# Kernel tuning notes

Measured on AMD Instinct MI355X. Metric: run time of the kernel, lower is better.

## Reference

```python
import jax, jax.numpy as jnp
import numpy as np


def conv2d(x, w, bias, stride=1, pad=0, groups=1):
    out = jax.lax.conv_general_dilated(
        x, w, (stride, stride), [(pad, pad), (pad, pad)],
        dimension_numbers=("NCHW", "OIHW", "NCHW"), feature_group_count=groups)
    return out + bias[None, :, None, None]


PATCHSIZE = [(4, 4), (8, 8)]
NEG = jnp.float32(-1e9)


def setup_inputs() -> dict:
    key = jax.random.key(0)
    ks = jax.random.split(key, 24)
    d = 128
    s = 0.05
    inp = {
        "x": jax.random.normal(ks[0], (16, d, 64, 64), jnp.float32),
        "m": jax.random.uniform(ks[1], (16, 1, 64, 64), jnp.float32),
        "depth_map": jax.random.normal(ks[2], (16, 1, 256, 256), jnp.float32),
        "wq": jax.random.normal(ks[3], (d, d, 1, 1), jnp.float32) * s,
        "bq": jax.random.normal(ks[4], (d,), jnp.float32) * s,
        "wk": jax.random.normal(ks[5], (d, d, 1, 1), jnp.float32) * s,
        "bk": jax.random.normal(ks[6], (d,), jnp.float32) * s,
        "wv": jax.random.normal(ks[7], (d, d, 1, 1), jnp.float32) * s,
        "bv": jax.random.normal(ks[8], (d,), jnp.float32) * s,
        "wvle": jax.random.normal(ks[9], (d, 1, 3, 3), jnp.float32) * s,  # depthwise
        "bvle": jax.random.normal(ks[10], (d,), jnp.float32) * s,
        "wd1": jax.random.normal(ks[11], (d, 1, 3, 3), jnp.float32) * s,
        "bd1": jax.random.normal(ks[12], (d,), jnp.float32) * s,
        "wd2": jax.random.normal(ks[13], (1, d, 3, 3), jnp.float32) * s,
        "bd2": jax.random.normal(ks[14], (1,), jnp.float32) * s,
        "wo": jax.random.normal(ks[15], (d, d, 3, 3), jnp.float32) * s,
        "bo": jax.random.normal(ks[16], (d,), jnp.float32) * s,
        "b": 2,
        "c": 128,
    }
    return inp


def _forward(x, m, depth_map, wq, bq, wk, bk, wv, bv, wvle, bvle,
             wd1, bd1, wd2, bd2, wo, bo, b, c):
    bt, _, h, w = x.shape
    t = bt // b
    d_k = c // len(PATCHSIZE)

    q_all = conv2d(x, wq, bq)
    k_all = conv2d(x, wk, bk)
    v_all = conv2d(x, wv, bv) + conv2d(x, wvle, bvle, pad=1, groups=c)
    d1 = jax.nn.relu(conv2d(depth_map, wd1, bd1, stride=2, pad=1))
    _depth = jax.nn.relu(conv2d(d1, wd2, bd2, stride=2, pad=1))  # (bt,1,h,w)

    outs = []
    for i, (width, height) in enumerate(PATCHSIZE):
        out_w, out_h = w // width, h // height
        L = t * out_h * out_w

        def patch(z, ch):
            # (b*t, ch, h, w) -> (b, L, ch*height*width)
            z = z.reshape(b, t, ch, out_h, height, out_w, width)
            return z.transpose(0, 1, 3, 5, 2, 4, 6).reshape(b, L, ch * height * width)

        mask = jnp.mean(patch(m, 1), -1) > 0.5            # (b, L) per-key mask
        dsort = jnp.sort(patch(_depth, 1), -1)            # (b, L, height*width)
        hw = height * width
        dmin, dmed, dmax = dsort[..., 0], dsort[..., (hw - 1) // 2], dsort[..., -1]

        q = patch(q_all[:, i * d_k:(i + 1) * d_k], d_k)
        k_ = patch(k_all[:, i * d_k:(i + 1) * d_k], d_k)
        v = patch(v_all[:, i * d_k:(i + 1) * d_k], d_k)

        scale = 1.0 / jnp.sqrt(jnp.float32(q.shape[-1]))
        s = jnp.einsum("bqd,bkd->bqk", q, k_) * scale     # shared QK^T

        def head(dbias):
            ss = s * jax.nn.sigmoid(dbias)[:, None, :]
            ss = jnp.where(mask[:, None, :], NEG, ss)
            return jnp.einsum("bqk,bkd->bqd", jax.nn.softmax(ss, -1), v)

        y = (head(dmed) + head(dmax) + head(dmin)) / 3.0
        y = y.reshape(b, t, out_h, out_w, d_k, height, width)
        y = y.transpose(0, 1, 4, 2, 5, 3, 6).reshape(bt, d_k, h, w)
        outs.append(y)

    out = jnp.concatenate(outs, 1)
    out = conv2d(out, wo, bo, pad=1)
    out = jnp.where(out >= 0, out, 0.2 * out)  # LeakyReLU(0.2)
    return out


def reference(x, m, depth_map, wq, bq, wk, bk, wv, bv, wvle, bvle,
              wd1, bd1, wd2, bd2, wo, bo, b, c):
    out = _forward(x, m, depth_map, wq, bq, wk, bk, wv, bv, wvle, bvle,
                   wd1, bd1, wd2, bd2, wo, bo, b, c)
    return (out, depth_map)
```

## Files before the change

### kernel.cpp

```cpp
#include <hip/hip_runtime.h>
#include <cmath>

typedef unsigned short u16;
typedef __attribute__((ext_vector_type(8))) __bf16 bf16x8;
typedef __attribute__((ext_vector_type(4))) float f32x4;

constexpr int Bb = 2, Tt = 8, Dc = 128, PIX = 4096;

__device__ inline u16 f2bf(float f) {
    unsigned u = __builtin_bit_cast(unsigned, f);
    u += 0x7fffu + ((u >> 16) & 1u);
    return (u16)(u >> 16);
}
__device__ inline float bf2f(u16 h) {
    unsigned u = ((unsigned)h) << 16;
    return __builtin_bit_cast(float, u);
}

#define GLOAD16(gp, lp) __builtin_amdgcn_global_load_lds( \
    (const __attribute__((address_space(1))) void*)(const void*)(gp), \
    (__attribute__((address_space(3))) void*)(void*)(lp), 16, 0, 0)

__device__ inline void mfma_chunk(const u16* lAs, const u16* lBs, int wave, int lane,
                                  f32x4 (&acc)[4][4])
{
    const int wm = (wave >> 1) * 64, wn = (wave & 1) * 64;
    const int fr = lane & 15;
    const int q4 = lane >> 4;
    const int sw = (q4 ^ ((fr >> 1) & 3)) * 8;
    bf16x8 av[4], bv[4];
#pragma unroll
    for (int i = 0; i < 4; ++i) av[i] = *(const bf16x8*)&lAs[(wm + i * 16 + fr) * 32 + sw];
#pragma unroll
    for (int j = 0; j < 4; ++j) bv[j] = *(const bf16x8*)&lBs[(wn + j * 16 + fr) * 32 + sw];
#pragma unroll
    for (int i = 0; i < 4; ++i)
#pragma unroll
        for (int j = 0; j < 4; ++j)
            acc[i][j] = __builtin_amdgcn_mfma_f32_16x16x32_bf16(av[i], bv[j], acc[i][j], 0, 0, 0);
}

__device__ inline void mfma_nt(const u16* A, int ldkA, const u16* B, int ldkB,
                               int kChunks, int wave, int lane,
                               u16* lAs, u16* lBs, f32x4 (&acc)[4][4])
{
    const int r = lane >> 2;
    const int kq8 = ((lane & 3) ^ ((r >> 1) & 3)) * 8;
    const u16* ga0 = A + (size_t)(wave * 32 + r) * ldkA + kq8;
    const u16* ga1 = ga0 + (size_t)16 * ldkA;
    const u16* gb0 = B + (size_t)(wave * 32 + r) * ldkB + kq8;
    const u16* gb1 = gb0 + (size_t)16 * ldkB;
    for (int kb = 0; kb < kChunks; ++kb) {
        __syncthreads();
        GLOAD16(ga0 + kb * 32, lAs + wave * 1024);
        GLOAD16(ga1 + kb * 32, lAs + wave * 1024 + 512);
        GLOAD16(gb0 + kb * 32, lBs + wave * 1024);
        GLOAD16(gb1 + kb * 32, lBs + wave * 1024 + 512);
        __syncthreads();
        mfma_chunk(lAs, lBs, wave, lane, acc);
    }
}

__global__ void k_prep(const float* __restrict__ wq, const float* __restrict__ wk,
                       const float* __restrict__ wv, const float* __restrict__ wo,
                       u16* __restrict__ Wqkv, u16* __restrict__ WoT)
{
    int idx = blockIdx.x * 256 + threadIdx.x;
    if (idx < 49152) {
        const float* w = idx < 16384 ? wq : (idx < 32768 ? wk : wv);
        Wqkv[idx] = f2bf(w[idx & 16383]);
    }
    int j = idx - 49152;
    if (j >= 0 && j < 147456) {
        int tap = j / 16384, rem = j % 16384;
        WoT[j] = f2bf(wo[(size_t)rem * 9 + tap]);
    }
}

__global__ __launch_bounds__(256) void k_xt(const float* __restrict__ x, u16* __restrict__ Xt)
{
    __shared__ float ls[128 * 65];
    const int n = blockIdx.y, pix0 = blockIdx.x * 64;
#pragma unroll
    for (int rep = 0; rep < 32; ++rep) {
        int idx = rep * 256 + threadIdx.x;
        int cin = idx >> 6, p = idx & 63;
        ls[cin * 65 + p] = x[((size_t)n * Dc + cin) * PIX + pix0 + p];
    }
    __syncthreads();
#pragma unroll
    for (int rep = 0; rep < 32; ++rep) {
        int idx = rep * 256 + threadIdx.x;
        int p = idx >> 7, cin = idx & 127;
        Xt[((size_t)n * PIX + pix0 + p) * Dc + cin] = f2bf(ls[cin * 65 + p]);
    }
}

__global__ __launch_bounds__(256) void k_qkv_mfma(const u16* __restrict__ Wqkv,
                                                  const u16* __restrict__ Xt,
                                                  const float* __restrict__ bq,
                                                  const float* __restrict__ bk,
                                                  const float* __restrict__ bv,
                                                  u16* __restrict__ Qp0, u16* __restrict__ Kp0,
                                                  u16* __restrict__ Qp1, u16* __restrict__ Kp1,
                                                  u16* __restrict__ v_bf)
{
    __shared__ u16 lAs[4096], lBs[4096];
    const int tid = threadIdx.x, wave = tid >> 6, lane = tid & 63;
    const int mt = blockIdx.y, n = blockIdx.z, px0 = blockIdx.x * 128;
    f32x4 acc[4][4];
#pragma unroll
    for (int i = 0; i < 4; ++i)
#pragma unroll
        for (int j = 0; j < 4; ++j) acc[i][j] = (f32x4){0.f, 0.f, 0.f, 0.f};
    mfma_nt(Wqkv + (size_t)mt * 128 * 128, 128,
            Xt + ((size_t)n * PIX + px0) * 128, 128, 4, wave, lane, lAs, lBs, acc);
    const int wm = (wave >> 1) * 64, wn = (wave & 1) * 64;
    const int rb = (lane >> 4) * 4, cb = lane & 15;
    const int bi = n >> 3, ti = n & 7;
    if (mt < 2) {
        const float* bp = (mt == 0) ? bq : bk;
        u16* d0 = (mt == 0) ? Qp0 : Kp0;
        u16* d1 = (mt == 0) ? Qp1 : Kp1;
#pragma unroll
        for (int i = 0; i < 4; ++i)
#pragma unroll
            for (int reg = 0; reg < 4; ++reg) {
                int c = wm + i * 16 + rb + reg;
                float bias = bp[c];
#pragma unroll
                for (int j = 0; j < 4; ++j) {
                    int pix = px0 + wn + j * 16 + cb;
                    int y = pix >> 6, x = pix & 63;
                    u16 val = f2bf(acc[i][j][reg] + bias);
                    if (c < 64) {
                        int l = ti * 256 + (y >> 2) * 16 + (x >> 2);
                        int f = c * 16 + (y & 3) * 4 + (x & 3);
                        d0[((size_t)bi * 2048 + l) * 1024 + f] = val;
                    } else {
                        int l = ti * 64 + (y >> 3) * 8 + (x >> 3);
                        int f = (c - 64) * 64 + (y & 7) * 8 + (x & 7);
                        d1[((size_t)bi * 512 + l) * 4096 + f] = val;
                    }
                }
            }
    } else {
#pragma unroll
        for (int i = 0; i < 4; ++i)
#pragma unroll
            for (int reg = 0; reg < 4; ++reg) {
                int c = wm + i * 16 + rb + reg;
                float bias = bv[c];
#pragma unroll
                for (int j = 0; j < 4; ++j) {
                    int pix = px0 + wn + j * 16 + cb;
                    v_bf[((size_t)n * Dc + c) * PIX + pix] = f2bf(acc[i][j][reg] + bias);
                }
            }
    }
}

__global__ __launch_bounds__(256) void k_vdw(const float* __restrict__ X,
                                             const float* __restrict__ wvle,
                                             const float* __restrict__ bvle,
                                             u16* __restrict__ v_bf)
{
    __shared__ float ls[4096];
    const int c = blockIdx.x, n = blockIdx.y;
    const int tid = threadIdx.x;
    const float* xp = X + ((size_t)n * Dc + c) * PIX;
#pragma unroll
    for (int r = 0; r < 4; ++r)
        *(float4*)&ls[r * 1024 + tid * 4] = *(const float4*)&xp[r * 1024 + tid * 4];
    __syncthreads();
    float w[9];
#pragma unroll
    for (int t = 0; t < 9; ++t) w[t] = wvle[c * 9 + t];
    const float bias = bvle[c];
    const int x = tid & 63, y0 = (tid >> 6) * 16;
    const bool xl = (x > 0), xr = (x < 63);
    u16* vp = v_bf + ((size_t)n * Dc + c) * PIX;
#pragma unroll
    for (int r = 0; r < 16; ++r) {
        int y = y0 + r;
        float s = bias;
#pragma unroll
        for (int ky = 0; ky < 3; ++ky) {
            int yy = y + ky - 1;
            if (yy < 0 || yy > 63) continue;
            const float* row = &ls[yy * 64];
            float m  = row[x];
            float lv = xl ? row[x - 1] : 0.f;
            float rv = xr ? row[x + 1] : 0.f;
            s += w[ky * 3 + 0] * lv + w[ky * 3 + 1] * m + w[ky * 3 + 2] * rv;
        }
        int idx = y * 64 + x;
        vp[idx] = f2bf(bf2f(vp[idx]) + s);
    }
}

__global__ __launch_bounds__(256) void k_d1(const float* __restrict__ dm,
                                            const float* __restrict__ wd1,
                                            const float* __restrict__ bd1,
                                            u16* __restrict__ d1b)
{
    __shared__ float ls[17 * 132];
    const int n = blockIdx.y;
    const int yt = blockIdx.x >> 1, xh = blockIdx.x & 1;
    const int Y0 = yt * 8;
    const int tid = threadIdx.x;
    const float* dmp = dm + (size_t)n * 65536;
    for (int idx = tid; idx < 17 * 132; idx += 256) {
        int row = idx / 132, cl = idx % 132;
        int gr = 2 * Y0 - 1 + row;
        int gc = 128 * xh - 1 + cl;
        float v = 0.f;
        if (gr >= 0 && gr < 256 && gc >= 0 && gc < 256 && cl < 129) v = dmp[gr * 256 + gc];
        ls[idx] = v;
    }
    __syncthreads();
    const int Xl = tid & 63;
    const int Yl0 = tid >> 6;
    float in0[9], in1[9];
#pragma unroll
    for (int jy = 0; jy < 3; ++jy)
#pragma unroll
        for (int jx = 0; jx < 3; ++jx) {
            in0[jy * 3 + jx] = ls[(2 * Yl0 + jy) * 132 + 2 * Xl + jx];
            in1[jy * 3 + jx] = ls[(2 * (Yl0 + 4) + jy) * 132 + 2 * Xl + jx];
        }
    const int X = 64 * xh + Xl;
    u16* outbase = d1b + (size_t)n * Dc * 16384 + (size_t)Y0 * 128 + X;
    for (int c = 0; c < 128; ++c) {
        const float* w1 = wd1 + c * 9;
        float a0 = bd1[c], a1 = a0;
#pragma unroll
        for (int t = 0; t < 9; ++t) { a0 += w1[t] * in0[t]; a1 += w1[t] * in1[t]; }
        u16* ob = outbase + (size_t)c * 16384;
        ob[(size_t)Yl0 * 128]       = f2bf(fmaxf(a0, 0.f));
        ob[(size_t)(Yl0 + 4) * 128] = f2bf(fmaxf(a1, 0.f));
    }
}

__global__ __launch_bounds__(256) void k_d2p(const u16* __restrict__ d1b,
                                             const float* __restrict__ wd2,
                                             float* __restrict__ part)
{
    __shared__ u16 ls[33 * 136];
    const int yt = blockIdx.x, n = blockIdx.y, cg = blockIdx.z;
    const int tid = threadIdx.x;
    const int y0 = yt * 16;
    if (tid < 33) ls[tid * 136 + 7] = 0;
    const int x = tid & 63;
    const int yl0 = (tid >> 6) * 4;
    float acc[4] = {0.f, 0.f, 0.f, 0.f};
    for (int c = 0; c < 16; ++c) {
        const u16* src = d1b + ((size_t)n * Dc + cg * 16 + c) * 16384;
        __syncthreads();
        for (int idx = tid; idx < 33 * 16; idx += 256) {
            int row = idx >> 4, s = idx & 15;
            int gr = 2 * y0 - 1 + row;
            uint4 v = make_uint4(0, 0, 0, 0);
            if (gr >= 0 && gr < 128) v = *(const uint4*)(src + gr * 128 + s * 8);
            *(uint4*)&ls[row * 136 + 8 + s * 8] = v;
        }
        __syncthreads();
        const float* w2 = wd2 + (cg * 16 + c) * 9;
        float w[9];
#pragma unroll
        for (int t = 0; t < 9; ++t) w[t] = w2[t];
#pragma unroll
        for (int r = 0; r < 4; ++r) {
            int yl = yl0 + r;
#pragma unroll
            for (int ky = 0; ky < 3; ++ky) {
                const u16* rp = &ls[(2 * yl + ky) * 136 + 2 * x + 7];
                float v0 = bf2f(rp[0]);
                unsigned pr = *(const unsigned*)(rp + 1);
                float v1 = bf2f((u16)(pr & 0xffffu));
                float v2 = bf2f((u16)(pr >> 16));
                acc[r] += w[ky * 3 + 0] * v0 + w[ky * 3 + 1] * v1 + w[ky * 3 + 2] * v2;
            }
        }
    }
    float* pp = part + ((size_t)cg * 16 + n) * PIX;
#pragma unroll
    for (int r = 0; r < 4; ++r)
        pp[(y0 + yl0 + r) * 64 + x] = acc[r];
}

__global__ void k_dfin(const float* __restrict__ part, const float* __restrict__ bd2,
                       float* __restrict__ dep)
{
    int idx = blockIdx.x * 256 + threadIdx.x;
    float s = bd2[0];
#pragma unroll
    for (int cg = 0; cg < 8; ++cg) s += part[(size_t)cg * 65536 + idx];
    dep[idx] = fmaxf(s, 0.f);
}

template<int PS>
__global__ __launch_bounds__(256) void k_stats2(const float* __restrict__ mI,
                                                const float* __restrict__ dep,
                                                float* __restrict__ maskf,
                                                float* __restrict__ smed,
                                                float* __restrict__ smaxA,
                                                float* __restrict__ sminA,
                                                int outn, int L)
{
    constexpr int HW = PS * PS;
    constexpr int TPB = 256 / HW;
    const int tok = blockIdx.x * TPB + threadIdx.x / HW;
    const int el  = threadIdx.x % HW;
    if (tok >= Bb * L) return;
    const int bi = tok / L, l = tok % L;
    const int ti = l / (outn * outn); const int rem = l % (outn * outn);
    const int oh = rem / outn, ow = rem % outn;
    const int n = bi * Tt + ti;
    const int py = el / PS, px = el % PS;
    const size_t off = (size_t)n * PIX + (size_t)(oh * PS + py) * 64 + ow * PS + px;
    const float mv = mI[off];
    const float dv = dep[off];
    float msum = mv, vmin = dv, vmax = dv;
#pragma unroll
    for (int o = HW / 2; o > 0; o >>= 1) {
        msum += __shfl_xor(msum, o);
        vmin = fminf(vmin, __shfl_xor(vmin, o));
        vmax = fmaxf(vmax, __shfl_xor(vmax, o));
    }
    const int gbase = (threadIdx.x & 63) & ~(HW - 1);
    int cl = 0, ce = 0;
#pragma unroll
    for (int b2 = 0; b2 < HW; ++b2) {
        float vb = __shfl(dv, gbase + b2);
        cl += (vb < dv);
        ce += (vb == dv);
    }
    constexpr int kk = (HW - 1) / 2;
    if (el == 0) {
        maskf[tok] = (msum / (float)HW > 0.5f) ? 1.f : 0.f;
        smaxA[tok] = 1.f / (1.f + __expf(-vmax));
        sminA[tok] = 1.f / (1.f + __expf(-vmin));
    }
    if (cl <= kk && kk < cl + ce)
        smed[tok] = 1.f / (1.f + __expf(-dv));
}

__global__ void k_patchT(const u16* __restrict__ v_bf, u16* __restrict__ Vt,
                         int ps, int outn, int L, int F, int cbase)
{
    size_t idx = (size_t)blockIdx.x * 256 + threadIdx.x;
    size_t total = (size_t)Bb * F * L / 4;
    if (idx >= total) return;
    int l0 = (int)((idx * 4) % L);
    size_t t2 = (idx * 4) / L;
    int f = (int)(t2 % F);
    int bi = (int)(t2 / F);
    int hw = ps * ps;
    int c = cbase + f / hw, r = f % hw;
    int py = r / ps, px = r % ps;
    int ti = l0 / (outn * outn); int rem = l0 % (outn * outn);
    int oh = rem / outn, ow0 = rem % outn;
    size_t base = ((size_t)(bi * Tt + ti) * Dc + c) * PIX + (oh * ps + py) * 64 + px;
    u16 out4[4];
#pragma unroll
    for (int e = 0; e < 4; ++e) out4[e] = v_bf[base + (size_t)(ow0 + e) * ps];
    *(uint2*)&Vt[((size_t)bi * F + f) * L + l0] = *(uint2*)out4;
}

__global__ __launch_bounds__(256) void k_qkT_mfma(const u16* __restrict__ Qp,
                                                  const u16* __restrict__ Kp,
                                                  u16* __restrict__ S,
                                                  int L, int F, int ksplit, float scale)
{
    __shared__ u16 lAs[4096], lBs[4096];
    const int tid = threadIdx.x, wave = tid >> 6, lane = tid & 63;
    const int bi = blockIdx.z / ksplit, ks = blockIdx.z % ksplit;
    const int kf = F / ksplit;
    f32x4 acc[4][4];
#pragma unroll
    for (int i = 0; i < 4; ++i)
#pragma unroll
        for (int j = 0; j < 4; ++j) acc[i][j] = (f32x4){0.f, 0.f, 0.f, 0.f};
    mfma_nt(Qp + (size_t)bi * L * F + (size_t)blockIdx.y * 128 * F + (size_t)ks * kf, F,
            Kp + (size_t)bi * L * F + (size_t)blockIdx.x * 128 * F + (size_t)ks * kf, F,
            kf / 32, wave, lane, lAs, lBs, acc);
    const int wm = (wave >> 1) * 64, wn = (wave & 1) * 64;
    const int rb = (lane >> 4) * 4, cb = lane & 15;
    u16* Cp = S + ((size_t)ks * Bb + bi) * L * L;
#pragma unroll
    for (int i = 0; i < 4; ++i)
#pragma unroll
        for (int reg = 0; reg < 4; ++reg) {
            int gm = blockIdx.y * 128 + wm + i * 16 + rb + reg;
#pragma unroll
            for (int j = 0; j < 4; ++j) {
                int gn = blockIdx.x * 128 + wn + j * 16 + cb;
                Cp[(size_t)gm * L + gn] = f2bf(acc[i][j][reg] * scale);
            }
        }
}

__device__ inline float blockMax(float v, float* sh) {
#pragma unroll
    for (int o = 32; o > 0; o >>= 1) v = fmaxf(v, __shfl_down(v, o));
    __syncthreads();
    if ((threadIdx.x & 63) == 0) sh[threadIdx.x >> 6] = v;
    __syncthreads();
    return fmaxf(fmaxf(sh[0], sh[1]), fmaxf(sh[2], sh[3]));
}
__device__ inline float blockSum(float v, float* sh) {
#pragma unroll
    for (int o = 32; o > 0; o >>= 1) v += __shfl_down(v, o);
    __syncthreads();
    if ((threadIdx.x & 63) == 0) sh[threadIdx.x >> 6] = v;
    __syncthreads();
    return sh[0] + sh[1] + sh[2] + sh[3];
}

template<int NV, int NSPLIT>
__global__ __launch_bounds__(256) void k_softmax(const u16* __restrict__ S,
                                                 u16* __restrict__ Pb,
                                                 const float* __restrict__ maskf,
                                                 const float* __restrict__ smed,
                                                 const float* __restrict__ smaxA,
                                                 const float* __restrict__ sminA,
                                                 int L)
{
    __shared__ float sred[4];
    const int bi = blockIdx.y, q = blockIdx.x;
    const size_t pstr = (size_t)Bb * L * L;
    const u16* row = S + (size_t)bi * L * L + (size_t)q * L;
    u16* prow = Pb + (size_t)bi * L * L + (size_t)q * L;
    const float* mk  = maskf + bi * L;
    const float* s0p = smed  + bi * L;
    const float* s1p = smaxA + bi * L;
    const float* s2p = sminA + bi * L;
    const int tid = threadIdx.x;
    float a0[NV], a1[NV], a2[NV];
    float m0 = -3.4e38f, m1 = -3.4e38f, m2 = -3.4e38f;
#pragma unroll
    for (int e = 0; e < NV; ++e) {
        int k = e * 256 + tid;
        float sv = bf2f(row[k]);
#pragma unroll
        for (int s2 = 1; s2 < NSPLIT; ++s2) sv += bf2f(row[(size_t)s2 * pstr + k]);
        bool msk = mk[k] > 0.5f;
        float v0 = msk ? -1e9f : sv * s0p[k];
        float v1 = msk ? -1e9f : sv * s1p[k];
        float v2 = msk ? -1e9f : sv * s2p[k];
        a0[e] = v0; a1[e] = v1; a2[e] = v2;
        m0 = fmaxf(m0, v0); m1 = fmaxf(m1, v1); m2 = fmaxf(m2, v2);
    }
    m0 = blockMax(m0, sred); m1 = blockMax(m1, sred); m2 = blockMax(m2, sred);
    float l0 = 0.f, l1 = 0.f, l2 = 0.f;
#pragma unroll
    for (int e = 0; e < NV; ++e) {
        a0[e] = __expf(a0[e] - m0); l0 += a0[e];
        a1[e] = __expf(a1[e] - m1); l1 += a1[e];
        a2[e] = __expf(a2[e] - m2); l2 += a2[e];
    }
    l0 = blockSum(l0, sred); l1 = blockSum(l1, sred); l2 = blockSum(l2, sred);
    float c0 = 1.f / (3.f * l0), c1 = 1.f / (3.f * l1), c2 = 1.f / (3.f * l2);
#pragma unroll
    for (int e = 0; e < NV; ++e)
        prow[e * 256 + tid] = f2bf(a0[e] * c0 + a1[e] * c1 + a2[e] * c2);
}

__global__ __launch_bounds__(256) void k_pv_mfma(const u16* __restrict__ Pb,
                                                 const u16* __restrict__ Vt,
                                                 u16* __restrict__ Yp,
                                                 int L, int F, int ksplit)
{
    __shared__ u16 lAs[4096], lBs[4096];
    const int tid = threadIdx.x, wave = tid >> 6, lane = tid & 63;
    const int bi = blockIdx.z / ksplit, ks = blockIdx.z % ksplit;
    const int kf = L / ksplit;
    f32x4 acc[4][4];
#pragma unroll
    for (int i = 0; i < 4; ++i)
#pragma unroll
        for (int j = 0; j < 4; ++j) acc[i][j] = (f32x4){0.f, 0.f, 0.f, 0.f};
    mfma_nt(Pb + (size_t)bi * L * L + (size_t)blockIdx.y * 128 * L + (size_t)ks * kf, L,
            Vt + (size_t)bi * F * L + (size_t)blockIdx.x * 128 * L + (size_t)ks * kf, L,
            kf / 32, wave, lane, lAs, lBs, acc);
    const int wm = (wave >> 1) * 64, wn = (wave & 1) * 64;
    const int rb = (lane >> 4) * 4, cb = lane & 15;
    u16* Cp = Yp + ((size_t)(ks * Bb + bi) * L) * F;
#pragma unroll
    for (int i = 0; i < 4; ++i)
#pragma unroll
        for (int reg = 0; reg < 4; ++reg) {
            int gm = blockIdx.y * 128 + wm + i * 16 + rb + reg;
#pragma unroll
            for (int j = 0; j < 4; ++j) {
                int gn = blockIdx.x * 128 + wn + j * 16 + cb;
                Cp[(size_t)gm * F + gn] = f2bf(acc[i][j][reg]);
            }
        }
}

template<int NSPLIT>
__global__ void k_unpatch(const u16* __restrict__ Yp, u16* __restrict__ catbT,
                          int ps, int outn, int L, int F, int cbase)
{
    size_t idx = (size_t)blockIdx.x * 256 + threadIdx.x;
    size_t total = (size_t)Bb * L * F / 4;
    if (idx >= total) return;
    const size_t pstr = (size_t)Bb * L * F;
    int f0 = (int)((idx * 4) % F);
    size_t t2 = (idx * 4) / F;
    int l = (int)(t2 % L);
    int bi = (int)(t2 / L);
    size_t off = ((size_t)bi * L + l) * F + f0;
    float s[4] = {0.f, 0.f, 0.f, 0.f};
#pragma unroll
    for (int sp = 0; sp < NSPLIT; ++sp) {
        uint2 u = *(const uint2*)&Yp[(size_t)sp * pstr + off];
        s[0] += bf2f((u16)(u.x & 0xffffu));
        s[1] += bf2f((u16)(u.x >> 16));
        s[2] += bf2f((u16)(u.y & 0xffffu));
        s[3] += bf2f((u16)(u.y >> 16));
    }
    int hw = ps * ps;
    int c = cbase + f0 / hw, r0 = f0 % hw;
    int ti = l / (outn * outn); int rem = l % (outn * outn);
    int oh = rem / outn, ow = rem % outn;
    int n = bi * Tt + ti;
    int py = r0 / ps, px = r0 % ps;
    size_t base = ((size_t)n * PIX + (size_t)(oh * ps + py) * 64 + ow * ps + px) * Dc + c;
#pragma unroll
    for (int e = 0; e < 4; ++e)
        catbT[base + (size_t)e * Dc] = f2bf(s[e]);
}

__global__ __launch_bounds__(256) void k_conv_mfma(const u16* __restrict__ catbT,
                                                   const u16* __restrict__ WoT,
                                                   const u16* __restrict__ zp,
                                                   u16* __restrict__ Cpart)
{
    __shared__ u16 lAs[4096], lBs[4096];
    const int tid = threadIdx.x, wave = tid >> 6, lane = tid & 63;
    const int pix0 = blockIdx.x * 128;
    const int sp = blockIdx.y;
    const int r = lane >> 2;
    const int kq8 = ((lane & 3) ^ ((r >> 1) & 3)) * 8;
    int yb[2], xb[2], nn[2];
#pragma unroll
    for (int s = 0; s < 2; ++s) {
        int pg = pix0 + wave * 32 + r + s * 16;
        nn[s] = pg >> 12; yb[s] = (pg >> 6) & 63; xb[s] = pg & 63;
    }
    const u16* gb_base = WoT + (size_t)(wave * 32 + r) * 128 + kq8;
    f32x4 acc[4][4];
#pragma unroll
    for (int i = 0; i < 4; ++i)
#pragma unroll
        for (int j = 0; j < 4; ++j) acc[i][j] = (f32x4){0.f, 0.f, 0.f, 0.f};
    for (int t = sp * 18; t < sp * 18 + 18; ++t) {
        const int tap = t >> 2, kc = t & 3;
        const int dy = tap / 3 - 1, dx = tap % 3 - 1;
        const u16* ga[2];
#pragma unroll
        for (int s = 0; s < 2; ++s) {
            int y = yb[s] + dy, xx = xb[s] + dx;
            bool ok = ((unsigned)y < 64u) && ((unsigned)xx < 64u);
            ga[s] = ok ? catbT + (((size_t)(nn[s] << 12) + y * 64 + xx) << 7) + kq8 + kc * 32 : zp;
        }
        const u16* gb = gb_base + tap * 16384 + kc * 32;
        __syncthreads();
        GLOAD16(ga[0], lAs + wave * 1024);
        GLOAD16(ga[1], lAs + wave * 1024 + 512);
        GLOAD16(gb, lBs + wave * 1024);
        GLOAD16(gb + 2048, lBs + wave * 1024 + 512);
        __syncthreads();
        mfma_chunk(lAs, lBs, wave, lane, acc);
    }
    const int wm = (wave >> 1) * 64, wn = (wave & 1) * 64;
    const int rb = (lane >> 4) * 4, cb = lane & 15;
    u16* Cp = Cpart + (size_t)sp * 8388608;
#pragma unroll
    for (int i = 0; i < 4; ++i)
#pragma unroll
        for (int reg = 0; reg < 4; ++reg) {
            int gm = pix0 + wm + i * 16 + rb + reg;
#pragma unroll
            for (int j = 0; j < 4; ++j) {
                int gn = wn + j * 16 + cb;
                Cp[(size_t)gm * 128 + gn] = f2bf(acc[i][j][reg]);
            }
        }
}

__global__ __launch_bounds__(256) void k_cfin(const u16* __restrict__ Cpart,
                                              const float* __restrict__ bo,
                                              float* __restrict__ outp)
{
    const int pg0 = blockIdx.x * 64;
    const int lane = threadIdx.x & 63, wv = threadIdx.x >> 6;
    const int pix = pg0 + lane;
    const int n = pix >> 12, p = pix & 4095;
    const u16* r0 = Cpart + (size_t)pix * 128 + wv * 32;
    const u16* r1 = r0 + 8388608;
#pragma unroll
    for (int c4 = 0; c4 < 8; ++c4) {
        uint2 a = *(const uint2*)(r0 + c4 * 4);
        uint2 b = *(const uint2*)(r1 + c4 * 4);
        float s[4];
        s[0] = bf2f((u16)(a.x & 0xffffu)) + bf2f((u16)(b.x & 0xffffu));
        s[1] = bf2f((u16)(a.x >> 16))     + bf2f((u16)(b.x >> 16));
        s[2] = bf2f((u16)(a.y & 0xffffu)) + bf2f((u16)(b.y & 0xffffu));
        s[3] = bf2f((u16)(a.y >> 16))     + bf2f((u16)(b.y >> 16));
#pragma unroll
        for (int e = 0; e < 4; ++e) {
            int cout = wv * 32 + c4 * 4 + e;
            float v = s[e] + bo[cout];
            v = (v >= 0.f) ? v : 0.2f * v;
            outp[((size_t)n * Dc + cout) * PIX + p] = v;
        }
    }
}

extern "C" void kernel_launch(void* const* d_in, const int* in_sizes, int n_in,
                              void* d_out, int out_size, void* d_ws, size_t ws_size,
                              hipStream_t stream)
{
    (void)in_sizes; (void)n_in; (void)out_size; (void)ws_size;
    const float* x    = (const float*)d_in[0];
    const float* mI   = (const float*)d_in[1];
    const float* dmap = (const float*)d_in[2];
    const float* wq   = (const float*)d_in[3];
    const float* bq   = (const float*)d_in[4];
    const float* wk   = (const float*)d_in[5];
    const float* bk   = (const float*)d_in[6];
    const float* wv   = (const float*)d_in[7];
    const float* bv   = (const float*)d_in[8];
    const float* wvle = (const float*)d_in[9];
    const float* bvle = (const float*)d_in[10];
    const float* wd1  = (const float*)d_in[11];
    const float* bd1  = (const float*)d_in[12];
    const float* wd2  = (const float*)d_in[13];
    const float* bd2  = (const float*)d_in[14];
    const float* wo   = (const float*)d_in[15];
    const float* bo   = (const float*)d_in[16];

    char* w8 = (char*)d_ws;
    u16*   v_bf  = (u16*)(w8);
    u16*   Xt    = (u16*)(w8 + 0x1000000);
    u16*   catbT = (u16*)(w8 + 0x2000000);
    u16*   Qp0   = (u16*)(w8 + 0x3000000);
    u16*   Kp0   = (u16*)(w8 + 0x3800000);
    u16*   Qp1   = (u16*)(w8 + 0x4000000);
    u16*   Kp1   = (u16*)(w8 + 0x4800000);
    u16*   Vt    = (u16*)(w8 + 0x5000000);
    u16*   Sb    = (u16*)(w8 + 0x5800000);
    u16*   Pb    = (u16*)(w8 + 0x7800000);
    u16*   Yp    = (u16*)(w8 + 0x8800000);
    u16*   Cpart = (u16*)(w8 + 0x5800000);
    u16*   d1b   = (u16*)(w8 + 0x3000000);
    float* dep   = (float*)(w8 + 0xA800000);
    float* maskf = (float*)(w8 + 0xA840000);
    float* smed  = (float*)(w8 + 0xA844000);
    float* smaxA = (float*)(w8 + 0xA848000);
    float* sminA = (float*)(w8 + 0xA84C000);
    u16*   Wqkv  = (u16*)(w8 + 0xA850000);
    u16*   WoT   = (u16*)(w8 + 0xA868000);
    u16*   zp    = (u16*)(w8 + 0xA8B0000);
    float* part  = (float*)(w8 + 0xA8C0000);
    float* outp  = (float*)d_out;

    hipMemcpyAsync(outp + 8388608, dmap, (size_t)16 * 65536 * sizeof(float),
                   hipMemcpyDeviceToDevice, stream);
    hipMemsetAsync(zp, 0, 256, stream);

    dim3 blk(256);
    k_d1<<<dim3(32, 16), blk, 0, stream>>>(dmap, wd1, bd1, d1b);
    k_d2p<<<dim3(4, 16, 8), blk, 0, stream>>>(d1b, wd2, part);
    k_dfin<<<dim3(256), blk, 0, stream>>>(part, bd2, dep);

    k_prep<<<dim3(768), blk, 0, stream>>>(wq, wk, wv, wo, Wqkv, WoT);
    k_xt<<<dim3(64, 16), blk, 0, stream>>>(x, Xt);
    k_qkv_mfma<<<dim3(32, 3, 16), blk, 0, stream>>>(Wqkv, Xt, bq, bk, bv,
                                                    Qp0, Kp0, Qp1, Kp1, v_bf);
    k_vdw<<<dim3(128, 16), blk, 0, stream>>>(x, wvle, bvle, v_bf);

    for (int i = 0; i < 2; ++i) {
        const int ps = (i == 0) ? 4 : 8;
        const int outn = 64 / ps;
        const int L = Tt * outn * outn;
        const int F = 64 * ps * ps;
        const int cbase = i * 64;
        const float scale = 1.0f / sqrtf((float)F);
        const int ksplit  = (i == 0) ? 2 : 16;
        const int pvsplit = 4;
        const u16* Qp = (i == 0) ? Qp0 : Qp1;
        const u16* Kp = (i == 0) ? Kp0 : Kp1;

        if (i == 0) k_stats2<4><<<dim3(Bb * L * 16 / 256), blk, 0, stream>>>(mI, dep, maskf, smed, smaxA, sminA, outn, L);
        else        k_stats2<8><<<dim3(Bb * L * 64 / 256), blk, 0, stream>>>(mI, dep, maskf, smed, smaxA, sminA, outn, L);

        const int pgrid = (int)(((size_t)Bb * L * F / 4 + 255) / 256);
        k_patchT<<<dim3(pgrid), blk, 0, stream>>>(v_bf, Vt, ps, outn, L, F, cbase);

        k_qkT_mfma<<<dim3(L / 128, L / 128, Bb * ksplit), blk, 0, stream>>>(Qp, Kp, Sb, L, F, ksplit, scale);

        if (i == 0) k_softmax<8, 2><<<dim3(L, Bb), blk, 0, stream>>>(Sb, Pb, maskf, smed, smaxA, sminA, L);
        else        k_softmax<2, 16><<<dim3(L, Bb), blk, 0, stream>>>(Sb, Pb, maskf, smed, smaxA, sminA, L);

        k_pv_mfma<<<dim3(F / 128, L / 128, Bb * pvsplit), blk, 0, stream>>>(Pb, Vt, Yp, L, F, pvsplit);
        k_unpatch<4><<<dim3(pgrid), blk, 0, stream>>>(Yp, catbT, ps, outn, L, F, cbase);
    }

    k_conv_mfma<<<dim3(512, 2), blk, 0, stream>>>(catbT, WoT, zp, Cpart);
    k_cfin<<<dim3(1024), blk, 0, stream>>>(Cpart, bo, outp);
}
```

Before: 464.3 us.

## Process two K-chunks per barrier pair in MFMA GEMMs and vectorize softmax rows

Each GEMM main loop (shared mfma_nt and the conv kernel) now loads two 32-wide K-chunks into doubled LDS buffers per sync pair and runs two MFMA chunks, halving the barrier count and increasing loads in flight. Softmax switches to contiguous per-thread element ownership, reading bf16 pairs as 32-bit words and writing the row with wide vector stores. The doubled LDS footprint may reduce occupancy, and the mfma_nt loop assumes an even number of chunks.

Result: slower. 475.7 us (+2.5%).

```diff
diff --git a/kernel.cpp b/kernel.cpp
--- a/kernel.cpp
+++ b/kernel.cpp
@@ -50,14 +50,19 @@
     const u16* ga1 = ga0 + (size_t)16 * ldkA;
     const u16* gb0 = B + (size_t)(wave * 32 + r) * ldkB + kq8;
     const u16* gb1 = gb0 + (size_t)16 * ldkB;
-    for (int kb = 0; kb < kChunks; ++kb) {
+    for (int kb = 0; kb < kChunks; kb += 2) {
         __syncthreads();
         GLOAD16(ga0 + kb * 32, lAs + wave * 1024);
         GLOAD16(ga1 + kb * 32, lAs + wave * 1024 + 512);
         GLOAD16(gb0 + kb * 32, lBs + wave * 1024);
         GLOAD16(gb1 + kb * 32, lBs + wave * 1024 + 512);
+        GLOAD16(ga0 + (kb + 1) * 32, lAs + 4096 + wave * 1024);
+        GLOAD16(ga1 + (kb + 1) * 32, lAs + 4096 + wave * 1024 + 512);
+        GLOAD16(gb0 + (kb + 1) * 32, lBs + 4096 + wave * 1024);
+        GLOAD16(gb1 + (kb + 1) * 32, lBs + 4096 + wave * 1024 + 512);
         __syncthreads();
         mfma_chunk(lAs, lBs, wave, lane, acc);
+        mfma_chunk(lAs + 4096, lBs + 4096, wave, lane, acc);
     }
 }
 
@@ -105,7 +110,7 @@
                                                   u16* __restrict__ Qp1, u16* __restrict__ Kp1,
                                                   u16* __restrict__ v_bf)
 {
-    __shared__ u16 lAs[4096], lBs[4096];
+    __shared__ u16 lAs[8192], lBs[8192];
     const int tid = threadIdx.x, wave = tid >> 6, lane = tid & 63;
     const int mt = blockIdx.y, n = blockIdx.z, px0 = blockIdx.x * 128;
     f32x4 acc[4][4];
@@ -373,7 +378,7 @@
                                                   u16* __restrict__ S,
                                                   int L, int F, int ksplit, float scale)
 {
-    __shared__ u16 lAs[4096], lBs[4096];
+    __shared__ u16 lAs[8192], lBs[8192];
     const int tid = threadIdx.x, wave = tid >> 6, lane = tid & 63;
     const int bi = blockIdx.z / ksplit, ks = blockIdx.z % ksplit;
     const int kf = F / ksplit;
@@ -437,20 +442,33 @@
     const float* s1p = smaxA + bi * L;
     const float* s2p = sminA + bi * L;
     const int tid = threadIdx.x;
+    const int k0 = tid * NV;
     float a0[NV], a1[NV], a2[NV];
     float m0 = -3.4e38f, m1 = -3.4e38f, m2 = -3.4e38f;
 #pragma unroll
-    for (int e = 0; e < NV; ++e) {
-        int k = e * 256 + tid;
-        float sv = bf2f(row[k]);
-#pragma unroll
-        for (int s2 = 1; s2 < NSPLIT; ++s2) sv += bf2f(row[(size_t)s2 * pstr + k]);
-        bool msk = mk[k] > 0.5f;
-        float v0 = msk ? -1e9f : sv * s0p[k];
-        float v1 = msk ? -1e9f : sv * s1p[k];
-        float v2 = msk ? -1e9f : sv * s2p[k];
-        a0[e] = v0; a1[e] = v1; a2[e] = v2;
-        m0 = fmaxf(m0, v0); m1 = fmaxf(m1, v1); m2 = fmaxf(m2, v2);
+    for (int e = 0; e < NV; e += 2) {
+        int k = k0 + e;
+        unsigned u = *(const unsigned*)&row[k];
+        float sva = bf2f((u16)(u & 0xffffu));
+        float svb = bf2f((u16)(u >> 16));
+#pragma unroll
+        for (int s2 = 1; s2 < NSPLIT; ++s2) {
+            unsigned w = *(const unsigned*)&row[(size_t)s2 * pstr + k];
+            sva += bf2f((u16)(w & 0xffffu));
+            svb += bf2f((u16)(w >> 16));
+        }
+        float sv2[2] = {sva, svb};
+#pragma unroll
+        for (int c2 = 0; c2 < 2; ++c2) {
+            int kc = k + c2;
+            bool msk = mk[kc] > 0.5f;
+            float sv = sv2[c2];
+            float v0 = msk ? -1e9f : sv * s0p[kc];
+            float v1 = msk ? -1e9f : sv * s1p[kc];
+            float v2 = msk ? -1e9f : sv * s2p[kc];
+            a0[e + c2] = v0; a1[e + c2] = v1; a2[e + c2] = v2;
+            m0 = fmaxf(m0, v0); m1 = fmaxf(m1, v1); m2 = fmaxf(m2, v2);
+        }
     }
     m0 = blockMax(m0, sred); m1 = blockMax(m1, sred); m2 = blockMax(m2, sred);
     float l0 = 0.f, l1 = 0.f, l2 = 0.f;
@@ -462,9 +480,16 @@
     }
     l0 = blockSum(l0, sred); l1 = blockSum(l1, sred); l2 = blockSum(l2, sred);
     float c0 = 1.f / (3.f * l0), c1 = 1.f / (3.f * l1), c2 = 1.f / (3.f * l2);
+    u16 outv[NV];
 #pragma unroll
     for (int e = 0; e < NV; ++e)
-        prow[e * 256 + tid] = f2bf(a0[e] * c0 + a1[e] * c1 + a2[e] * c2);
+        outv[e] = f2bf(a0[e] * c0 + a1[e] * c1 + a2[e] * c2);
+    if (NV == 8)      *(uint4*)&prow[k0] = *(uint4*)outv;
+    else if (NV == 2) *(unsigned*)&prow[k0] = *(unsigned*)outv;
+    else {
+#pragma unroll
+        for (int e = 0; e < NV; ++e) prow[k0 + e] = outv[e];
+    }
 }
 
 __global__ __launch_bounds__(256) void k_pv_mfma(const u16* __restrict__ Pb,
@@ -472,7 +497,7 @@
                                                  u16* __restrict__ Yp,
                                                  int L, int F, int ksplit)
 {
-    __shared__ u16 lAs[4096], lBs[4096];
+    __shared__ u16 lAs[8192], lBs[8192];
     const int tid = threadIdx.x, wave = tid >> 6, lane = tid & 63;
     const int bi = blockIdx.z / ksplit, ks = blockIdx.z % ksplit;
     const int kf = L / ksplit;
@@ -539,7 +564,7 @@
                                                    const u16* __restrict__ zp,
                                                    u16* __restrict__ Cpart)
 {
-    __shared__ u16 lAs[4096], lBs[4096];
+    __shared__ u16 lAs[8192], lBs[8192];
     const int tid = threadIdx.x, wave = tid >> 6, lane = tid & 63;
     const int pix0 = blockIdx.x * 128;
     const int sp = blockIdx.y;
@@ -557,24 +582,30 @@
     for (int i = 0; i < 4; ++i)
 #pragma unroll
         for (int j = 0; j < 4; ++j) acc[i][j] = (f32x4){0.f, 0.f, 0.f, 0.f};
-    for (int t = sp * 18; t < sp * 18 + 18; ++t) {
-        const int tap = t >> 2, kc = t & 3;
-        const int dy = tap / 3 - 1, dx = tap % 3 - 1;
-        const u16* ga[2];
-#pragma unroll
-        for (int s = 0; s < 2; ++s) {
-            int y = yb[s] + dy, xx = xb[s] + dx;
-            bool ok = ((unsigned)y < 64u) && ((unsigned)xx < 64u);
-            ga[s] = ok ? catbT + (((size_t)(nn[s] << 12) + y * 64 + xx) << 7) + kq8 + kc * 32 : zp;
-        }
-        const u16* gb = gb_base + tap * 16384 + kc * 32;
+    for (int tp = 0; tp < 9; ++tp) {
+        const int t0 = sp * 18 + tp * 2;
         __syncthreads();
-        GLOAD16(ga[0], lAs + wave * 1024);
-        GLOAD16(ga[1], lAs + wave * 1024 + 512);
-        GLOAD16(gb, lBs + wave * 1024);
-        GLOAD16(gb + 2048, lBs + wave * 1024 + 512);
+#pragma unroll
+        for (int h = 0; h < 2; ++h) {
+            const int t = t0 + h;
+            const int tap = t >> 2, kc = t & 3;
+            const int dy = tap / 3 - 1, dx = tap % 3 - 1;
+            const u16* ga[2];
+#pragma unroll
+            for (int s = 0; s < 2; ++s) {
+                int y = yb[s] + dy, xx = xb[s] + dx;
+                bool ok = ((unsigned)y < 64u) && ((unsigned)xx < 64u);
+                ga[s] = ok ? catbT + (((size_t)(nn[s] << 12) + y * 64 + xx) << 7) + kq8 + kc * 32 : zp;
+            }
+            const u16* gb = gb_base + tap * 16384 + kc * 32;
+            GLOAD16(ga[0], lAs + h * 4096 + wave * 1024);
+            GLOAD16(ga[1], lAs + h * 4096 + wave * 1024 + 512);
+            GLOAD16(gb, lBs + h * 4096 + wave * 1024);
+            GLOAD16(gb + 2048, lBs + h * 4096 + wave * 1024 + 512);
+        }
         __syncthreads();
         mfma_chunk(lAs, lBs, wave, lane, acc);
+        mfma_chunk(lAs + 4096, lBs + 4096, wave, lane, acc);
     }
     const int wm = (wave >> 1) * 64, wn = (wave & 1) * 64;
     const int rb = (lane >> 4) * 4, cb = lane & 15;
```
